# Optimization experiments

Hardware: AMD Instinct MI355X
Metric: run time of the kernel (lower is better)

The kernel has to match this reference:

```python
import jax, jax.numpy as jnp
import numpy as np

B, T, C, H = 2, 2048, 1024, 16
HS = C // H  # head size = 64


def setup_inputs() -> dict:
    key = jax.random.key(0)
    k1, k2, k3 = jax.random.split(key, 3)
    X = jax.random.normal(k1, (B, T, C), dtype=jnp.float32)
    W_qkv = jax.random.normal(k2, (C, 3 * C), dtype=jnp.float32) * (C ** -0.5)
    W_proj = jax.random.normal(k3, (C, C), dtype=jnp.float32) * (C ** -0.5)
    return {"X": X, "W_qkv": W_qkv, "W_proj": W_proj}


def reference(X, W_qkv, W_proj):
    b, t, c = X.shape
    h, hs = H, c // H
    qkv = X @ W_qkv                      # [b,t,3c]
    k_, q_, v_ = jnp.split(qkv, 3, axis=2)  # module order: K, Q, V
    K = k_.reshape(b, t, h, hs).transpose(0, 2, 1, 3)  # [b,h,t,hs]
    Q = q_.reshape(b, t, h, hs).transpose(0, 2, 1, 3)
    V = v_.reshape(b, t, h, hs).transpose(0, 2, 1, 3)
    # NOTE: original scales by full embed dim c**-0.5 (not head_size)
    scores = jnp.einsum('bhqd,bhkd->bhqk', Q, K) * (c ** -0.5)
    causal = jnp.tril(jnp.ones((t, t), dtype=bool))
    scores = jnp.where(causal, scores, -jnp.inf)
    W = jax.nn.softmax(scores, axis=-1)  # dropout is identity in eval mode
    out = jnp.einsum('bhqk,bhkd->bhqd', W, V)  # [b,h,t,hs]
    out = out.transpose(0, 2, 1, 3).reshape(b, t, c)
    return out @ W_proj
```

## Files before the change

kernel.cpp:

```cpp
#include <hip/hip_runtime.h>

#define TB 2
#define TT 2048
#define TC 1024
#define TH 16
#define THS 64

typedef short bf16x8 __attribute__((ext_vector_type(8)));
typedef float f32x4 __attribute__((ext_vector_type(4)));

#define QSCALE 0.0450842200278f

__device__ inline unsigned short f2b(float f) {
    unsigned u = __builtin_bit_cast(unsigned, f);
    unsigned r = (u + 0x7fffu + ((u >> 16) & 1u)) >> 16;
    return (unsigned short)r;
}
__device__ inline unsigned short f2b_hw(float f) {
    __bf16 h = (__bf16)f;
    return __builtin_bit_cast(unsigned short, h);
}
__device__ inline float b2f(unsigned short h) {
    unsigned u = ((unsigned)h) << 16;
    return __builtin_bit_cast(float, u);
}

__device__ inline void gl_lds16(const unsigned short* g, unsigned short* l) {
    __builtin_amdgcn_global_load_lds(
        (const __attribute__((address_space(1))) unsigned int*)(g),
        (__attribute__((address_space(3))) unsigned int*)(l), 16, 0, 0);
}

__device__ inline float dpp_sum16(float x) {
    int t;
    t = __builtin_amdgcn_update_dpp(0, __builtin_bit_cast(int, x), 0x128, 0xf, 0xf, true);
    x += __builtin_bit_cast(float, t);
    t = __builtin_amdgcn_update_dpp(0, __builtin_bit_cast(int, x), 0x124, 0xf, 0xf, true);
    x += __builtin_bit_cast(float, t);
    t = __builtin_amdgcn_update_dpp(0, __builtin_bit_cast(int, x), 0x122, 0xf, 0xf, true);
    x += __builtin_bit_cast(float, t);
    t = __builtin_amdgcn_update_dpp(0, __builtin_bit_cast(int, x), 0x121, 0xf, 0xf, true);
    x += __builtin_bit_cast(float, t);
    return x;
}

__global__ void cvt_bf16_k(const float* __restrict__ in, unsigned short* __restrict__ out) {
    const int i = blockIdx.x * blockDim.x + threadIdx.x;
    const float4* p = (const float4*)in + (size_t)i * 2;
    const float4 a = p[0], b = p[1];
    bf16x8 v;
    v[0] = (short)f2b(a.x); v[1] = (short)f2b(a.y);
    v[2] = (short)f2b(a.z); v[3] = (short)f2b(a.w);
    v[4] = (short)f2b(b.x); v[5] = (short)f2b(b.y);
    v[6] = (short)f2b(b.z); v[7] = (short)f2b(b.w);
    *(bf16x8*)(out + (size_t)i * 8) = v;
}

__global__ void transpose_cvt_k(const float* __restrict__ in,
                                unsigned short* __restrict__ out, int R, int Cc) {
    __shared__ float tile[32][33];
    const int tx = threadIdx.x, ty = threadIdx.y;
    const int r0 = blockIdx.y * 32, c0 = blockIdx.x * 32;
#pragma unroll
    for (int i = 0; i < 4; i++)
        tile[ty + i * 8][tx] = in[(size_t)(r0 + ty + i * 8) * Cc + c0 + tx];
    __syncthreads();
#pragma unroll
    for (int i = 0; i < 4; i++)
        out[(size_t)(c0 + ty + i * 8) * R + r0 + tx] = f2b(tile[tx][ty + i * 8]);
}

__global__ void vt_k(const unsigned short* __restrict__ Vb,
                     unsigned short* __restrict__ Vt) {
    __shared__ unsigned short tile[32][33];
    const int tx = threadIdx.x, ty = threadIdx.y;
    const int d0 = blockIdx.x * 32, t0 = blockIdx.y * 32, bh = blockIdx.z;
    const unsigned short* src = Vb + (size_t)bh * TT * THS;
    unsigned short* dst = Vt + (size_t)bh * THS * TT;
#pragma unroll
    for (int i = 0; i < 4; i++)
        tile[ty + i * 8][tx] = src[(size_t)(t0 + ty + i * 8) * THS + d0 + tx];
    __syncthreads();
#pragma unroll
    for (int i = 0; i < 4; i++)
        dst[(size_t)(d0 + ty + i * 8) * TT + t0 + tx] = tile[tx][ty + i * 8];
}

__global__ __launch_bounds__(256) void gemm_qkv(
    const unsigned short* __restrict__ A, const unsigned short* __restrict__ Bt, int K,
    unsigned short* __restrict__ outK, unsigned short* __restrict__ outQ,
    unsigned short* __restrict__ outV) {
    __shared__ __align__(16) unsigned short As[128 * 32];
    __shared__ __align__(16) unsigned short Bs[128 * 32];

    const int tid = threadIdx.x;
    const int wave = tid >> 6, lane = tid & 63;
    const int quad = lane >> 4, l16 = lane & 15;
    const int wm = (wave >> 1) * 64, wn = (wave & 1) * 64;
    const int m0 = blockIdx.y * 128, n0 = blockIdx.x * 128;

    const f32x4 vzero = {0.f, 0.f, 0.f, 0.f};
    f32x4 acc[4][4];
#pragma unroll
    for (int i = 0; i < 4; i++)
#pragma unroll
        for (int j = 0; j < 4; j++) acc[i][j] = vzero;

    const int nk = K >> 5;
    for (int kt = 0; kt < nk; ++kt) {
        const int k0 = kt * 32;
        __syncthreads();
#pragma unroll
        for (int it = 0; it < 2; ++it) {
            const int chunk = tid + it * 256;
            const int r = chunk >> 2, col = (chunk & 3) * 8;
            gl_lds16(A + (size_t)(m0 + r) * K + k0 + col, &As[chunk * 8]);
            gl_lds16(Bt + (size_t)(n0 + r) * K + k0 + col, &Bs[chunk * 8]);
        }
        __syncthreads();
        bf16x8 af[4], bfr[4];
#pragma unroll
        for (int f = 0; f < 4; ++f) {
            af[f] = *(const bf16x8*)(&As[(wm + f * 16 + l16) * 32 + quad * 8]);
            bfr[f] = *(const bf16x8*)(&Bs[(wn + f * 16 + l16) * 32 + quad * 8]);
        }
#pragma unroll
        for (int fm = 0; fm < 4; ++fm)
#pragma unroll
            for (int fn = 0; fn < 4; ++fn)
                acc[fm][fn] = __builtin_amdgcn_mfma_f32_16x16x32_bf16(
                    af[fm], bfr[fn], acc[fm][fn], 0, 0, 0);
    }

#pragma unroll
    for (int fm = 0; fm < 4; ++fm) {
#pragma unroll
        for (int fn = 0; fn < 4; ++fn) {
#pragma unroll
            for (int r = 0; r < 4; ++r) {
                const int row = m0 + wm + fm * 16 + quad * 4 + r;
                const int col = n0 + wn + fn * 16 + l16;
                const float val = acc[fm][fn][r];
                const int b = row >> 11, t = row & (TT - 1);
                const int chunkc = col >> 10, cc = col & (TC - 1);
                const int hh = cc >> 6, d = cc & 63;
                const size_t idx = (size_t)((b * TH + hh) * TT + t) * THS + d;
                if (chunkc == 0)
                    outK[idx] = f2b(val);
                else if (chunkc == 1)
                    outQ[idx] = f2b(val * QSCALE);
                else
                    outV[idx] = f2b(val);
            }
        }
    }
}

__global__ __launch_bounds__(256) void gemm_proj(
    const unsigned short* __restrict__ A, const unsigned short* __restrict__ Bt,
    int M, int N, int K, float* __restrict__ outF) {
    __shared__ __align__(16) unsigned short As[128 * 32];
    __shared__ __align__(16) unsigned short Bs[64 * 32];

    const int tid = threadIdx.x;
    const int wave = tid >> 6, lane = tid & 63;
    const int quad = lane >> 4, l16 = lane & 15;
    const int wm = wave * 32;
    const int m0 = blockIdx.y * 128, n0 = blockIdx.x * 64;

    const f32x4 vzero = {0.f, 0.f, 0.f, 0.f};
    f32x4 acc[2][4];
#pragma unroll
    for (int i = 0; i < 2; i++)
#pragma unroll
        for (int j = 0; j < 4; j++) acc[i][j] = vzero;

    const int nk = K >> 5;
    for (int kt = 0; kt < nk; ++kt) {
        const int k0 = kt * 32;
        __syncthreads();
#pragma unroll
        for (int it = 0; it < 2; ++it) {
            const int chunk = tid + it * 256;
            const int r = chunk >> 2, col = (chunk & 3) * 8;
            gl_lds16(A + (size_t)(m0 + r) * K + k0 + col, &As[chunk * 8]);
        }
        {
            const int r = tid >> 2, col = (tid & 3) * 8;
            gl_lds16(Bt + (size_t)(n0 + r) * K + k0 + col, &Bs[tid * 8]);
        }
        __syncthreads();
        bf16x8 af[2], bfr[4];
#pragma unroll
        for (int f = 0; f < 2; ++f)
            af[f] = *(const bf16x8*)(&As[(wm + f * 16 + l16) * 32 + quad * 8]);
#pragma unroll
        for (int f = 0; f < 4; ++f)
            bfr[f] = *(const bf16x8*)(&Bs[(f * 16 + l16) * 32 + quad * 8]);
#pragma unroll
        for (int fm = 0; fm < 2; ++fm)
#pragma unroll
            for (int fn = 0; fn < 4; ++fn)
                acc[fm][fn] = __builtin_amdgcn_mfma_f32_16x16x32_bf16(
                    af[fm], bfr[fn], acc[fm][fn], 0, 0, 0);
    }

#pragma unroll
    for (int fm = 0; fm < 2; ++fm)
#pragma unroll
        for (int fn = 0; fn < 4; ++fn)
#pragma unroll
            for (int r = 0; r < 4; ++r) {
                const int row = m0 + wm + fm * 16 + quad * 4 + r;
                const int col = n0 + fn * 16 + l16;
                outF[(size_t)row * N + col] = acc[fm][fn][r];
            }
}

__global__ __launch_bounds__(256, 3) void attn_k(
    const unsigned short* __restrict__ Qb, const unsigned short* __restrict__ Kb,
    const unsigned short* __restrict__ Vt, unsigned short* __restrict__ AO) {
    __shared__ __align__(16) unsigned short U[4][2304];
    __shared__ float lS[4][32];

    const int tid = threadIdx.x;
    const int w = tid >> 6, lane = tid & 63;
    const int quad = lane >> 4, l16 = lane & 15;
    const int bh = blockIdx.x;
    const int qtt = 63 - blockIdx.y;
    const int q0 = qtt * 32;
    const unsigned short* Qh = Qb + (size_t)bh * TT * THS;
    const unsigned short* Kh = Kb + (size_t)bh * TT * THS;
    const unsigned short* Vh = Vt + (size_t)bh * THS * TT;

    bf16x8 aQ[2][2];
#pragma unroll
    for (int rt = 0; rt < 2; ++rt)
#pragma unroll
        for (int ks = 0; ks < 2; ++ks)
            aQ[rt][ks] = *(const bf16x8*)(
                Qh + (size_t)(q0 + rt * 16 + l16) * THS + ks * 32 + quad * 8);

    const float NEGINF = -__builtin_inff();
    const f32x4 vzero = {0.f, 0.f, 0.f, 0.f};
    f32x4 o[2][4];
    float lp[2][4];
#pragma unroll
    for (int rt = 0; rt < 2; ++rt)
#pragma unroll
        for (int i = 0; i < 4; i++) { o[rt][i] = vzero; lp[rt][i] = 0.f; }

    const int nkt = (qtt >> 1) + 1;

    bf16x8 bK[8];
    {
        const int t0p = (w < nkt ? w : 0) * 64;
#pragma unroll
        for (int nt = 0; nt < 4; ++nt)
#pragma unroll
            for (int ks = 0; ks < 2; ++ks)
                bK[nt * 2 + ks] = *(const bf16x8*)(
                    Kh + (size_t)(t0p + nt * 16 + l16) * THS + ks * 32 + quad * 8);
    }

    for (int kt = w; kt < nkt; kt += 4) {
        const int t0 = kt * 64;
        bf16x8 bV[8];
#pragma unroll
        for (int nt = 0; nt < 4; ++nt)
#pragma unroll
            for (int ks = 0; ks < 2; ++ks)
                bV[nt * 2 + ks] = *(const bf16x8*)(
                    Vh + (size_t)(nt * 16 + l16) * TT + t0 + ks * 32 + quad * 8);
        const bool needmask = (kt == nkt - 1);
#pragma unroll
        for (int rt = 0; rt < 2; ++rt) {
            f32x4 s[4];
#pragma unroll
            for (int nt = 0; nt < 4; ++nt) s[nt] = vzero;
            __builtin_amdgcn_s_setprio(1);
#pragma unroll
            for (int ks = 0; ks < 2; ++ks)
#pragma unroll
                for (int nt = 0; nt < 4; ++nt)
                    s[nt] = __builtin_amdgcn_mfma_f32_16x16x32_bf16(
                        aQ[rt][ks], bK[nt * 2 + ks], s[nt], 0, 0, 0);
            __builtin_amdgcn_s_setprio(0);
            unsigned short* Pw = &U[w][0] + rt * 1152;
#pragma unroll
            for (int r = 0; r < 4; ++r) {
                const int row = q0 + rt * 16 + quad * 4 + r;
                float v0 = s[0][r], v1 = s[1][r], v2 = s[2][r], v3 = s[3][r];
                if (needmask) {
                    if (t0 + l16 > row) v0 = NEGINF;
                    if (t0 + 16 + l16 > row) v1 = NEGINF;
                    if (t0 + 32 + l16 > row) v2 = NEGINF;
                    if (t0 + 48 + l16 > row) v3 = NEGINF;
                }
                const float p0 = __builtin_amdgcn_exp2f(v0);
                const float p1 = __builtin_amdgcn_exp2f(v1);
                const float p2 = __builtin_amdgcn_exp2f(v2);
                const float p3 = __builtin_amdgcn_exp2f(v3);
                lp[rt][r] += (p0 + p1) + (p2 + p3);
                const int pr = (quad * 4 + r) * 72;
                Pw[pr + l16] = f2b_hw(p0);
                Pw[pr + 16 + l16] = f2b_hw(p1);
                Pw[pr + 32 + l16] = f2b_hw(p2);
                Pw[pr + 48 + l16] = f2b_hw(p3);
            }
        }
        asm volatile("s_waitcnt lgkmcnt(0)" ::: "memory");
        bf16x8 aP[2][2];
#pragma unroll
        for (int rt = 0; rt < 2; ++rt) {
            const unsigned short* Pw = &U[w][0] + rt * 1152;
            aP[rt][0] = *(const bf16x8*)(Pw + l16 * 72 + quad * 8);
            aP[rt][1] = *(const bf16x8*)(Pw + l16 * 72 + 32 + quad * 8);
        }
        bf16x8 nK[8];
        {
            const int t0n = (kt + 4 < nkt) ? t0 + 256 : t0;
#pragma unroll
            for (int nt = 0; nt < 4; ++nt)
#pragma unroll
                for (int ks = 0; ks < 2; ++ks)
                    nK[nt * 2 + ks] = *(const bf16x8*)(
                        Kh + (size_t)(t0n + nt * 16 + l16) * THS + ks * 32 + quad * 8);
        }
        __builtin_amdgcn_s_setprio(1);
#pragma unroll
        for (int rt = 0; rt < 2; ++rt)
#pragma unroll
            for (int ks = 0; ks < 2; ++ks)
#pragma unroll
                for (int nt = 0; nt < 4; ++nt)
                    o[rt][nt] = __builtin_amdgcn_mfma_f32_16x16x32_bf16(
                        aP[rt][ks], bV[nt * 2 + ks], o[rt][nt], 0, 0, 0);
        __builtin_amdgcn_s_setprio(0);
#pragma unroll
        for (int i = 0; i < 8; ++i) bK[i] = nK[i];
    }

#pragma unroll
    for (int rt = 0; rt < 2; ++rt)
#pragma unroll
        for (int r = 0; r < 4; ++r) {
            const float lsum = dpp_sum16(lp[rt][r]);
            const int row = rt * 16 + quad * 4 + r;
            if (l16 == 0) lS[w][row] = lsum;
#pragma unroll
            for (int nt = 0; nt < 4; ++nt)
                U[w][row * 66 + nt * 16 + l16] = f2b_hw(o[rt][nt][r]);
        }
    __syncthreads();

    const int b = bh >> 4, h = bh & 15;
    const int col = w * 16 + l16;
#pragma unroll
    for (int rr = 0; rr < 8; ++rr) {
        const int row = quad * 8 + rr;
        const float L = (lS[0][row] + lS[1][row]) + (lS[2][row] + lS[3][row]);
        const float O = (b2f(U[0][row * 66 + col]) + b2f(U[1][row * 66 + col])) +
                        (b2f(U[2][row * 66 + col]) + b2f(U[3][row * 66 + col]));
        const int t = q0 + row;
        AO[((size_t)(b * TT + t)) * TC + h * 64 + col] = f2b_hw(O * __builtin_amdgcn_rcpf(L));
    }
}

extern "C" void kernel_launch(void* const* d_in, const int* in_sizes, int n_in,
                              void* d_out, int out_size, void* d_ws, size_t ws_size,
                              hipStream_t stream) {
    const float* X = (const float*)d_in[0];
    const float* Wqkv = (const float*)d_in[1];
    const float* Wproj = (const float*)d_in[2];
    float* out = (float*)d_out;

    unsigned short* ws = (unsigned short*)d_ws;
    unsigned short* Xb = ws;
    unsigned short* Wq_t = Xb + 4096 * 1024;
    unsigned short* Wp_t = Wq_t + 3072 * 1024;
    unsigned short* Qb = Wp_t + 1024 * 1024;
    unsigned short* Kb = Qb + TB * TH * TT * THS;
    unsigned short* Vb = Kb + TB * TH * TT * THS;
    unsigned short* Vt = Vb + TB * TH * TT * THS;
    unsigned short* AO = Vt + TB * TH * TT * THS;

    cvt_bf16_k<<<dim3((4096 * 1024) / (8 * 256)), 256, 0, stream>>>(X, Xb);
    transpose_cvt_k<<<dim3(3072 / 32, 1024 / 32), dim3(32, 8), 0, stream>>>(Wqkv, Wq_t, 1024, 3072);
    transpose_cvt_k<<<dim3(1024 / 32, 1024 / 32), dim3(32, 8), 0, stream>>>(Wproj, Wp_t, 1024, 1024);
    gemm_qkv<<<dim3(3072 / 128, 4096 / 128), 256, 0, stream>>>(Xb, Wq_t, 1024, Kb, Qb, Vb);
    vt_k<<<dim3(THS / 32, TT / 32, TB * TH), dim3(32, 8), 0, stream>>>(Vb, Vt);
    attn_k<<<dim3(32, 64), 256, 0, stream>>>(Qb, Kb, Vt, AO);
    gemm_proj<<<dim3(1024 / 64, 4096 / 128), 256, 0, stream>>>(
        AO, Wp_t, 4096, 1024, 1024, out);
}
```

Baseline: 220.2 us.

## Share double-buffered K/V tiles in LDS across waves handling separate query rows

The attention kernel changes from four waves splitting the key range of one 32-row query tile to four waves each owning 32 query rows of a 128-row block. K and V tiles are staged into swizzled, double-buffered LDS with direct global-to-LDS loads, so one fetch of each tile serves all four waves. This removes the per-block cross-wave reduction of partial outputs and row sums, and reduces redundant global K/V reads. In exchange there is a block-wide barrier every tile, fewer and larger blocks (512 instead of 2048), and waves sit idle on causal tiles that lie beyond their own rows.

```diff
diff --git a/kernel.cpp b/kernel.cpp
--- a/kernel.cpp
+++ b/kernel.cpp
@@ -217,21 +217,23 @@
             }
 }
 
-__global__ __launch_bounds__(256, 3) void attn_k(
+__global__ __launch_bounds__(256) void attn_k(
     const unsigned short* __restrict__ Qb, const unsigned short* __restrict__ Kb,
     const unsigned short* __restrict__ Vt, unsigned short* __restrict__ AO) {
+    __shared__ __align__(16) unsigned short Ks[2][64 * 64];
+    __shared__ __align__(16) unsigned short Vs[2][64 * 64];
     __shared__ __align__(16) unsigned short U[4][2304];
-    __shared__ float lS[4][32];
 
     const int tid = threadIdx.x;
     const int w = tid >> 6, lane = tid & 63;
     const int quad = lane >> 4, l16 = lane & 15;
     const int bh = blockIdx.x;
-    const int qtt = 63 - blockIdx.y;
-    const int q0 = qtt * 32;
+    const int qb = 15 - blockIdx.y;
+    const int q0w = qb * 128 + w * 32;
     const unsigned short* Qh = Qb + (size_t)bh * TT * THS;
     const unsigned short* Kh = Kb + (size_t)bh * TT * THS;
     const unsigned short* Vh = Vt + (size_t)bh * THS * TT;
+    const int b = bh >> 4, h = bh & 15;
 
     bf16x8 aQ[2][2];
 #pragma unroll
@@ -239,7 +241,7 @@
 #pragma unroll
         for (int ks = 0; ks < 2; ++ks)
             aQ[rt][ks] = *(const bf16x8*)(
-                Qh + (size_t)(q0 + rt * 16 + l16) * THS + ks * 32 + quad * 8);
+                Qh + (size_t)(q0w + rt * 16 + l16) * THS + ks * 32 + quad * 8);
 
     const float NEGINF = -__builtin_inff();
     const f32x4 vzero = {0.f, 0.f, 0.f, 0.f};
@@ -250,121 +252,118 @@
 #pragma unroll
         for (int i = 0; i < 4; i++) { o[rt][i] = vzero; lp[rt][i] = 0.f; }
 
-    const int nkt = (qtt >> 1) + 1;
-
-    bf16x8 bK[8];
-    {
-        const int t0p = (w < nkt ? w : 0) * 64;
-#pragma unroll
-        for (int nt = 0; nt < 4; ++nt)
-#pragma unroll
-            for (int ks = 0; ks < 2; ++ks)
-                bK[nt * 2 + ks] = *(const bf16x8*)(
-                    Kh + (size_t)(t0p + nt * 16 + l16) * THS + ks * 32 + quad * 8);
-    }
-
-    for (int kt = w; kt < nkt; kt += 4) {
+    const int nkt = 2 * qb + 2;
+
+#pragma unroll
+    for (int it = 0; it < 2; ++it) {
+        const int c = tid + it * 256;
+        const int row = c >> 3, g = (c & 7) ^ (row & 7);
+        gl_lds16(Kh + (size_t)row * THS + g * 8, &Ks[0][c * 8]);
+        gl_lds16(Vh + (size_t)row * TT + g * 8, &Vs[0][c * 8]);
+    }
+    __syncthreads();
+
+    for (int kt = 0; kt < nkt; ++kt) {
         const int t0 = kt * 64;
-        bf16x8 bV[8];
-#pragma unroll
-        for (int nt = 0; nt < 4; ++nt)
-#pragma unroll
-            for (int ks = 0; ks < 2; ++ks)
-                bV[nt * 2 + ks] = *(const bf16x8*)(
-                    Vh + (size_t)(nt * 16 + l16) * TT + t0 + ks * 32 + quad * 8);
-        const bool needmask = (kt == nkt - 1);
-#pragma unroll
-        for (int rt = 0; rt < 2; ++rt) {
-            f32x4 s[4];
-#pragma unroll
-            for (int nt = 0; nt < 4; ++nt) s[nt] = vzero;
-            __builtin_amdgcn_s_setprio(1);
-#pragma unroll
-            for (int ks = 0; ks < 2; ++ks)
-#pragma unroll
-                for (int nt = 0; nt < 4; ++nt)
-                    s[nt] = __builtin_amdgcn_mfma_f32_16x16x32_bf16(
-                        aQ[rt][ks], bK[nt * 2 + ks], s[nt], 0, 0, 0);
-            __builtin_amdgcn_s_setprio(0);
-            unsigned short* Pw = &U[w][0] + rt * 1152;
-#pragma unroll
-            for (int r = 0; r < 4; ++r) {
-                const int row = q0 + rt * 16 + quad * 4 + r;
-                float v0 = s[0][r], v1 = s[1][r], v2 = s[2][r], v3 = s[3][r];
-                if (needmask) {
-                    if (t0 + l16 > row) v0 = NEGINF;
-                    if (t0 + 16 + l16 > row) v1 = NEGINF;
-                    if (t0 + 32 + l16 > row) v2 = NEGINF;
-                    if (t0 + 48 + l16 > row) v3 = NEGINF;
+        const int cur = kt & 1;
+        if (kt + 1 < nkt) {
+            const int t0n = t0 + 64;
+#pragma unroll
+            for (int it = 0; it < 2; ++it) {
+                const int c = tid + it * 256;
+                const int row = c >> 3, g = (c & 7) ^ (row & 7);
+                gl_lds16(Kh + (size_t)(t0n + row) * THS + g * 8, &Ks[cur ^ 1][c * 8]);
+                gl_lds16(Vh + (size_t)row * TT + t0n + g * 8, &Vs[cur ^ 1][c * 8]);
+            }
+        }
+        if (t0 <= q0w + 31) {
+            const unsigned short* Kc = &Ks[cur][0];
+            const unsigned short* Vc = &Vs[cur][0];
+            bf16x8 bK[8];
+#pragma unroll
+            for (int nt = 0; nt < 4; ++nt)
+#pragma unroll
+                for (int ks = 0; ks < 2; ++ks) {
+                    const int row = nt * 16 + l16;
+                    bK[nt * 2 + ks] = *(const bf16x8*)(
+                        Kc + row * 64 + (((ks * 4 + quad) ^ (row & 7)) * 8));
                 }
-                const float p0 = __builtin_amdgcn_exp2f(v0);
-                const float p1 = __builtin_amdgcn_exp2f(v1);
-                const float p2 = __builtin_amdgcn_exp2f(v2);
-                const float p3 = __builtin_amdgcn_exp2f(v3);
-                lp[rt][r] += (p0 + p1) + (p2 + p3);
-                const int pr = (quad * 4 + r) * 72;
-                Pw[pr + l16] = f2b_hw(p0);
-                Pw[pr + 16 + l16] = f2b_hw(p1);
-                Pw[pr + 32 + l16] = f2b_hw(p2);
-                Pw[pr + 48 + l16] = f2b_hw(p3);
-            }
-        }
-        asm volatile("s_waitcnt lgkmcnt(0)" ::: "memory");
-        bf16x8 aP[2][2];
-#pragma unroll
-        for (int rt = 0; rt < 2; ++rt) {
-            const unsigned short* Pw = &U[w][0] + rt * 1152;
-            aP[rt][0] = *(const bf16x8*)(Pw + l16 * 72 + quad * 8);
-            aP[rt][1] = *(const bf16x8*)(Pw + l16 * 72 + 32 + quad * 8);
-        }
-        bf16x8 nK[8];
-        {
-            const int t0n = (kt + 4 < nkt) ? t0 + 256 : t0;
+            const bool needmask = (t0 + 63 > q0w);
+#pragma unroll
+            for (int rt = 0; rt < 2; ++rt) {
+                f32x4 s[4];
+#pragma unroll
+                for (int nt = 0; nt < 4; ++nt) s[nt] = vzero;
+#pragma unroll
+                for (int ks = 0; ks < 2; ++ks)
+#pragma unroll
+                    for (int nt = 0; nt < 4; ++nt)
+                        s[nt] = __builtin_amdgcn_mfma_f32_16x16x32_bf16(
+                            aQ[rt][ks], bK[nt * 2 + ks], s[nt], 0, 0, 0);
+                unsigned short* Pw = &U[w][0] + rt * 1152;
+#pragma unroll
+                for (int r = 0; r < 4; ++r) {
+                    const int row = q0w + rt * 16 + quad * 4 + r;
+                    float v0 = s[0][r], v1 = s[1][r], v2 = s[2][r], v3 = s[3][r];
+                    if (needmask) {
+                        if (t0 + l16 > row) v0 = NEGINF;
+                        if (t0 + 16 + l16 > row) v1 = NEGINF;
+                        if (t0 + 32 + l16 > row) v2 = NEGINF;
+                        if (t0 + 48 + l16 > row) v3 = NEGINF;
+                    }
+                    const float p0 = __builtin_amdgcn_exp2f(v0);
+                    const float p1 = __builtin_amdgcn_exp2f(v1);
+                    const float p2 = __builtin_amdgcn_exp2f(v2);
+                    const float p3 = __builtin_amdgcn_exp2f(v3);
+                    lp[rt][r] += (p0 + p1) + (p2 + p3);
+                    const int pr = (quad * 4 + r) * 72;
+                    Pw[pr + l16] = f2b_hw(p0);
+                    Pw[pr + 16 + l16] = f2b_hw(p1);
+                    Pw[pr + 32 + l16] = f2b_hw(p2);
+                    Pw[pr + 48 + l16] = f2b_hw(p3);
+                }
+            }
+            asm volatile("s_waitcnt lgkmcnt(0)" ::: "memory");
+            bf16x8 aP[2][2];
+#pragma unroll
+            for (int rt = 0; rt < 2; ++rt) {
+                const unsigned short* Pw = &U[w][0] + rt * 1152;
+                aP[rt][0] = *(const bf16x8*)(Pw + l16 * 72 + quad * 8);
+                aP[rt][1] = *(const bf16x8*)(Pw + l16 * 72 + 32 + quad * 8);
+            }
+            bf16x8 bV[8];
 #pragma unroll
             for (int nt = 0; nt < 4; ++nt)
 #pragma unroll
+                for (int ks = 0; ks < 2; ++ks) {
+                    const int row = nt * 16 + l16;
+                    bV[nt * 2 + ks] = *(const bf16x8*)(
+                        Vc + row * 64 + (((ks * 4 + quad) ^ (row & 7)) * 8));
+                }
+#pragma unroll
+            for (int rt = 0; rt < 2; ++rt)
+#pragma unroll
                 for (int ks = 0; ks < 2; ++ks)
-                    nK[nt * 2 + ks] = *(const bf16x8*)(
-                        Kh + (size_t)(t0n + nt * 16 + l16) * THS + ks * 32 + quad * 8);
-        }
-        __builtin_amdgcn_s_setprio(1);
-#pragma unroll
-        for (int rt = 0; rt < 2; ++rt)
-#pragma unroll
-            for (int ks = 0; ks < 2; ++ks)
-#pragma unroll
-                for (int nt = 0; nt < 4; ++nt)
-                    o[rt][nt] = __builtin_amdgcn_mfma_f32_16x16x32_bf16(
-                        aP[rt][ks], bV[nt * 2 + ks], o[rt][nt], 0, 0, 0);
-        __builtin_amdgcn_s_setprio(0);
-#pragma unroll
-        for (int i = 0; i < 8; ++i) bK[i] = nK[i];
+#pragma unroll
+                    for (int nt = 0; nt < 4; ++nt)
+                        o[rt][nt] = __builtin_amdgcn_mfma_f32_16x16x32_bf16(
+                            aP[rt][ks], bV[nt * 2 + ks], o[rt][nt], 0, 0, 0);
+        }
+        __syncthreads();
     }
 
 #pragma unroll
     for (int rt = 0; rt < 2; ++rt)
 #pragma unroll
         for (int r = 0; r < 4; ++r) {
-            const float lsum = dpp_sum16(lp[rt][r]);
-            const int row = rt * 16 + quad * 4 + r;
-            if (l16 == 0) lS[w][row] = lsum;
+            const float L = dpp_sum16(lp[rt][r]);
+            const float rcpL = __builtin_amdgcn_rcpf(L);
+            const int t = q0w + rt * 16 + quad * 4 + r;
+            unsigned short* dst = AO + ((size_t)(b * TT + t)) * TC + h * 64;
 #pragma unroll
             for (int nt = 0; nt < 4; ++nt)
-                U[w][row * 66 + nt * 16 + l16] = f2b_hw(o[rt][nt][r]);
-        }
-    __syncthreads();
-
-    const int b = bh >> 4, h = bh & 15;
-    const int col = w * 16 + l16;
-#pragma unroll
-    for (int rr = 0; rr < 8; ++rr) {
-        const int row = quad * 8 + rr;
-        const float L = (lS[0][row] + lS[1][row]) + (lS[2][row] + lS[3][row]);
-        const float O = (b2f(U[0][row * 66 + col]) + b2f(U[1][row * 66 + col])) +
-                        (b2f(U[2][row * 66 + col]) + b2f(U[3][row * 66 + col]));
-        const int t = q0 + row;
-        AO[((size_t)(b * TT + t)) * TC + h * 64 + col] = f2b_hw(O * __builtin_amdgcn_rcpf(L));
-    }
+                dst[nt * 16 + l16] = f2b_hw(o[rt][nt][r] * rcpL);
+        }
 }
 
 extern "C" void kernel_launch(void* const* d_in, const int* in_sizes, int n_in,
@@ -390,7 +389,7 @@
     transpose_cvt_k<<<dim3(1024 / 32, 1024 / 32), dim3(32, 8), 0, stream>>>(Wproj, Wp_t, 1024, 1024);
     gemm_qkv<<<dim3(3072 / 128, 4096 / 128), 256, 0, stream>>>(Xb, Wq_t, 1024, Kb, Qb, Vb);
     vt_k<<<dim3(THS / 32, TT / 32, TB * TH), dim3(32, 8), 0, stream>>>(Vb, Vt);
-    attn_k<<<dim3(32, 64), 256, 0, stream>>>(Qb, Kb, Vt, AO);
+    attn_k<<<dim3(32, 16), 256, 0, stream>>>(Qb, Kb, Vt, AO);
     gemm_proj<<<dim3(1024 / 64, 4096 / 128), 256, 0, stream>>>(
         AO, Wp_t, 4096, 1024, 1024, out);
 }
```

Result: faster. 203.4 us (-7.6%).
